# Kernel optimization log

Hardware: AMD Instinct MI355X
Metric: run time of the kernel (lower is better)

Reference implementation:

```python
import jax, jax.numpy as jnp
import numpy as np

B, S, D, H = 4, 2048, 768, 12
DEPTH = D // H


def setup_inputs() -> dict:
    key = jax.random.key(0)
    ks = jax.random.split(key, 8)
    scale = 1.0 / np.sqrt(D)
    return {
        "v": jax.random.normal(ks[0], (B, S, D), jnp.float32),
        "k": jax.random.normal(ks[1], (B, S, D), jnp.float32),
        "q": jax.random.normal(ks[2], (B, S, D), jnp.float32),
        "wq": jax.random.normal(ks[3], (D, D), jnp.float32) * scale,
        "wk": jax.random.normal(ks[4], (D, D), jnp.float32) * scale,
        "wv": jax.random.normal(ks[5], (D, D), jnp.float32) * scale,
        "wo": jax.random.normal(ks[6], (D, D), jnp.float32) * scale,
        "bo": jax.random.normal(ks[7], (D,), jnp.float32) * 0.01,
    }


def _split_heads(x):
    # [B, S, D] -> [B, H, S, depth]
    return x.reshape(B, S, H, DEPTH).transpose(0, 2, 1, 3)


def reference(v, k, q, wq, wk, wv, wo, bo):
    # nn.Linear(bias=False): y = x @ W.T
    qh = _split_heads(q @ wq.T)
    kh = _split_heads(k @ wk.T)
    vh = _split_heads(v @ wv.T)
    # scaled dot-product attention (mask=None)
    logits = jnp.einsum("bhqd,bhkd->bhqk", qh, kh) / jnp.sqrt(
        jnp.asarray(DEPTH, jnp.float32)
    )
    attn = jax.nn.softmax(logits, axis=-1)  # [B, H, Sq, Sk]
    out = jnp.einsum("bhqk,bhkd->bhqd", attn, vh)
    concat = out.transpose(0, 2, 1, 3).reshape(B, S, D)
    return concat @ wo.T + bo
```

## Files before the change

kernel.cpp:

```cpp
#include <hip/hip_runtime.h>
#include <math.h>

#define BB 4
#define SS 2048
#define DD 768
#define HH 12
#define DEPTH 64
#define M_TOTAL (BB * SS)
#define WSZ (DD * DD)

typedef __attribute__((ext_vector_type(8))) short bf16x8;
typedef __attribute__((ext_vector_type(16))) float f32x16;
typedef __attribute__((ext_vector_type(4))) float f32x4;
typedef __attribute__((ext_vector_type(4))) unsigned short us4;
typedef __attribute__((ext_vector_type(2))) unsigned int u32x2;
typedef __attribute__((ext_vector_type(4))) unsigned int u32x4;

__device__ __forceinline__ unsigned short f2b(float f) {
  unsigned u = __builtin_bit_cast(unsigned, f);
  return (unsigned short)((u + 0x8000u) >> 16);
}

__device__ __forceinline__ unsigned pkrnd(float lo, float hi) {
  unsigned a = __builtin_bit_cast(unsigned, lo) + 0x8000u;
  unsigned b = __builtin_bit_cast(unsigned, hi) + 0x8000u;
  return __builtin_amdgcn_perm(b, a, 0x07060302);
}

__device__ __forceinline__ us4 f2b4(float a, float b, float c, float d) {
  unsigned lo = pkrnd(a, b), hi = pkrnd(c, d);
  us4 t;
  t.x = (unsigned short)lo; t.y = (unsigned short)(lo >> 16);
  t.z = (unsigned short)hi; t.w = (unsigned short)(hi >> 16);
  return t;
}

__device__ __forceinline__ float fexp2(float x) {
  return __builtin_amdgcn_exp2f(x);
}

#if __has_builtin(__builtin_amdgcn_permlane32_swap)
__device__ __forceinline__ void plswap(unsigned& a, unsigned& b) {
  u32x2 r = __builtin_amdgcn_permlane32_swap(a, b, false, false);
  a = r.x;
  b = r.y;
}
#else
__device__ __forceinline__ void plswap(unsigned& a, unsigned& b) {
  unsigned pa = (unsigned)__shfl_xor((int)a, 32, 64);
  unsigned pb = (unsigned)__shfl_xor((int)b, 32, 64);
  bool hi = ((threadIdx.x & 63) >> 5) != 0;
  unsigned na = hi ? pb : a;
  unsigned nb = hi ? b : pa;
  a = na;
  b = nb;
}
#endif

__device__ __forceinline__ void gl16(const void* g, void* l) {
  __builtin_amdgcn_global_load_lds(
      (const __attribute__((address_space(1))) unsigned int*)g,
      (__attribute__((address_space(3))) unsigned int*)l, 16, 0, 0);
}

__global__ __launch_bounds__(256) void prep(
    const float* __restrict__ s0, const float* __restrict__ s1,
    const float* __restrict__ s2, const float* __restrict__ s3,
    const float* __restrict__ s4, const float* __restrict__ s5,
    const float* __restrict__ s6, unsigned short* __restrict__ d0,
    unsigned short* __restrict__ d1, unsigned short* __restrict__ d2,
    unsigned short* __restrict__ d3, unsigned short* __restrict__ d4,
    unsigned short* __restrict__ d5, unsigned short* __restrict__ d6) {
  const float* s;
  unsigned short* d;
  int n;
  switch (blockIdx.y) {
    case 0: s = s0; d = d0; n = M_TOTAL * DD; break;
    case 1: s = s1; d = d1; n = M_TOTAL * DD; break;
    case 2: s = s2; d = d2; n = M_TOTAL * DD; break;
    case 3: s = s3; d = d3; n = WSZ; break;
    case 4: s = s4; d = d4; n = WSZ; break;
    case 5: s = s5; d = d5; n = WSZ; break;
    default: s = s6; d = d6; n = WSZ; break;
  }
  int idx = (blockIdx.x * 256 + threadIdx.x) * 4;
  if (idx >= n) return;
  float4 f = *(const float4*)(s + idx);
  *(us4*)(d + idx) = f2b4(f.x, f.y, f.z, f.w);
}

__global__ __launch_bounds__(256) void proj_qkv(
    const unsigned short* __restrict__ qb, const unsigned short* __restrict__ kb,
    const unsigned short* __restrict__ vb, const unsigned short* __restrict__ wqb,
    const unsigned short* __restrict__ wkb, const unsigned short* __restrict__ wvb,
    unsigned short* __restrict__ QF, unsigned short* __restrict__ KF,
    unsigned short* __restrict__ VF) {
  const int mode = blockIdx.z;
  const unsigned short* X;
  const unsigned short* W;
  if (mode == 0) { X = qb; W = wqb; }
  else if (mode == 1) { X = kb; W = wkb; }
  else { X = vb; W = wvb; }

  __shared__ __align__(16) char sm[34816];
  unsigned short* As = (unsigned short*)sm;
  unsigned short* Bs = (unsigned short*)(sm + 8192);
  unsigned short* Ts = (unsigned short*)sm;

  const int tid = threadIdx.x;
  const int lane = tid & 63, w_ = tid >> 6;
  const int lr = lane & 15, quad = lane >> 4;
  const int wm = (w_ & 1) * 64, wn = (w_ >> 1) * 64;
  const int m0 = blockIdx.x * 128, n0 = blockIdx.y * 128;
  const int grow = lane >> 2, gcol = (lane & 3) * 8;

  f32x4 acc[4][4];
#pragma unroll
  for (int mt = 0; mt < 4; ++mt)
#pragma unroll
    for (int nt = 0; nt < 4; ++nt) acc[mt][nt] = (f32x4){0.f, 0.f, 0.f, 0.f};

  for (int k0 = 0; k0 < DD; k0 += 32) {
    __syncthreads();
#pragma unroll
    for (int i = 0; i < 2; ++i) {
      int c = 4 * i + w_;
      int row = c * 16 + grow;
      gl16(X + (size_t)(m0 + row) * DD + k0 + gcol, (char*)As + c * 1024);
      gl16(W + (size_t)(n0 + row) * DD + k0 + gcol, (char*)Bs + c * 1024);
    }
    __syncthreads();

    bf16x8 af[4];
#pragma unroll
    for (int mt = 0; mt < 4; ++mt)
      af[mt] = *(const bf16x8*)&As[(wm + 16 * mt + lr) * 32 + 8 * quad];
#pragma unroll
    for (int nt = 0; nt < 4; ++nt) {
      bf16x8 bf = *(const bf16x8*)&Bs[(wn + 16 * nt + lr) * 32 + 8 * quad];
#pragma unroll
      for (int mt = 0; mt < 4; ++mt)
        acc[mt][nt] = __builtin_amdgcn_mfma_f32_16x16x32_bf16(af[mt], bf,
                                                              acc[mt][nt], 0, 0, 0);
    }
  }

  __syncthreads();

  const int b_ = m0 >> 11;
  const int hbase = n0 >> 6;
  const int sgbase = (m0 & 2047) >> 5;

  if (mode < 2) {
    const float osc = (mode == 0) ? 0.18033688011f : 1.0f;
#pragma unroll
    for (int mt = 0; mt < 4; ++mt)
#pragma unroll
      for (int nt = 0; nt < 4; ++nt) {
        int n = wn + 16 * nt + lr;
        int mb = wm + 16 * mt + 4 * quad;
#pragma unroll
        for (int r = 0; r < 4; ++r)
          Ts[(mb + r) * 136 + n] = f2b(acc[mt][nt][r] * osc);
      }
    __syncthreads();
    unsigned short* O = (mode == 0) ? QF : KF;
    const int ks = tid >> 6, lane2 = tid & 63;
    const int mrow = lane2 & 31, hb = lane2 >> 5;
#pragma unroll
    for (int c = 0; c < 8; ++c) {
      int hl = c >> 2, sblk = c & 3;
      int bh = b_ * HH + hbase + hl;
      bf16x8 vv = *(const bf16x8*)&Ts[(sblk * 32 + mrow) * 136 + hl * 64 +
                                      ks * 16 + hb * 8];
      *(bf16x8*)(O + ((size_t)bh * 64 + sgbase + sblk) * 2048 + tid * 8) = vv;
    }
  } else {
#pragma unroll
    for (int mt = 0; mt < 4; ++mt)
#pragma unroll
      for (int nt = 0; nt < 4; ++nt) {
        int n = wn + 16 * nt + lr;
        int mb = wm + 16 * mt + 4 * quad;
        *(us4*)&Ts[n * 136 + mb] =
            f2b4(acc[mt][nt][0], acc[mt][nt][1], acc[mt][nt][2], acc[mt][nt][3]);
      }
    __syncthreads();
    const int ntv = tid >> 7, ks2 = (tid >> 6) & 1, lane2 = tid & 63;
#pragma unroll
    for (int c = 0; c < 8; ++c) {
      int hl = c >> 2, sblk = c & 3;
      int bh = b_ * HH + hbase + hl;
      bf16x8 vv = *(const bf16x8*)&Ts[(hl * 64 + ntv * 32 + (lane2 & 31)) * 136 +
                                      sblk * 32 + ks2 * 16 + (lane2 >> 5) * 8];
      *(bf16x8*)(VF + ((size_t)bh * 64 + sgbase + sblk) * 2048 + tid * 8) = vv;
    }
  }
}

struct KV {
  bf16x8 k[4];
  bf16x8 v[4];
};

__global__ __launch_bounds__(256) void attn(
    const unsigned short* __restrict__ QF, const unsigned short* __restrict__ KF,
    const unsigned short* __restrict__ VF, unsigned short* __restrict__ cc) {
  __shared__ __align__(16) char smem[19200];
  float (*Osh)[64][36] = (float (*)[64][36])smem;
  float (*Ls)[2][32] = (float (*)[2][32])(smem + 18432);
  float (*Linv)[32] = (float (*)[32])(smem + 18944);

  const int tid = threadIdx.x;
  const int lane = tid & 63, w_ = tid >> 6;
  const int wq = w_ & 1, wk = w_ >> 1;
  const int m32 = lane & 31, h = lane >> 5;
  const int bh = blockIdx.x % 48;
  const int q0 = (blockIdx.x / 48) * 64;
  const size_t perbh = (size_t)SS * DEPTH;

  const unsigned short* qfb = QF + (size_t)bh * perbh;
  const unsigned short* kfb = KF + (size_t)bh * perbh + (size_t)wk * 2048 + lane * 8;
  const unsigned short* vfb = VF + (size_t)bh * perbh + (size_t)wk * 2048 + lane * 8;

  bf16x8 qf[4];
  {
    const unsigned short* p = qfb + (size_t)((q0 >> 5) + wq) * 2048 + lane * 8;
#pragma unroll
    for (int ks = 0; ks < 4; ++ks) qf[ks] = *(const bf16x8*)(p + ks * 512);
  }

  f32x16 o[2];
#pragma unroll
  for (int nt = 0; nt < 2; ++nt)
#pragma unroll
    for (int r = 0; r < 16; ++r) o[nt][r] = 0.f;
  float l_lane = 0.f;

#define LOADKV(tile, dst)                                                    \
  do {                                                                       \
    const unsigned short* kp_ = kfb + (size_t)(tile) * 4096;                 \
    const unsigned short* vp_ = vfb + (size_t)(tile) * 4096;                 \
    _Pragma("unroll") for (int x_ = 0; x_ < 4; ++x_) {                       \
      (dst).k[x_] = *(const bf16x8*)(kp_ + x_ * 512);                        \
      (dst).v[x_] = *(const bf16x8*)(vp_ + x_ * 512);                        \
    }                                                                        \
  } while (0)

#define TILECOMP(kv)                                                         \
  do {                                                                       \
    f32x16 st;                                                               \
    _Pragma("unroll") for (int r_ = 0; r_ < 16; ++r_) st[r_] = 0.f;          \
    _Pragma("unroll") for (int ks_ = 0; ks_ < 4; ++ks_)                      \
        st = __builtin_amdgcn_mfma_f32_32x32x16_bf16((kv).k[ks_], qf[ks_],   \
                                                     st, 0, 0, 0);           \
    float e_[16];                                                            \
    _Pragma("unroll") for (int r_ = 0; r_ < 16; ++r_) {                      \
      e_[r_] = fexp2(st[r_]);                                                \
      l_lane += e_[r_];                                                      \
    }                                                                        \
    unsigned p_[8];                                                          \
    _Pragma("unroll") for (int g_ = 0; g_ < 8; ++g_)                         \
        p_[g_] = pkrnd(e_[2 * g_], e_[2 * g_ + 1]);                          \
    plswap(p_[0], p_[2]);                                                    \
    plswap(p_[1], p_[3]);                                                    \
    plswap(p_[4], p_[6]);                                                    \
    plswap(p_[5], p_[7]);                                                    \
    u32x4 fa_ = {p_[0], p_[1], p_[2], p_[3]};                                \
    u32x4 fb_ = {p_[4], p_[5], p_[6], p_[7]};                                \
    bf16x8 pa1 = __builtin_bit_cast(bf16x8, fa_);                            \
    bf16x8 pa2 = __builtin_bit_cast(bf16x8, fb_);                            \
    o[0] = __builtin_amdgcn_mfma_f32_32x32x16_bf16(pa1, (kv).v[0], o[0], 0, 0, 0); \
    o[1] = __builtin_amdgcn_mfma_f32_32x32x16_bf16(pa1, (kv).v[2], o[1], 0, 0, 0); \
    o[0] = __builtin_amdgcn_mfma_f32_32x32x16_bf16(pa2, (kv).v[1], o[0], 0, 0, 0); \
    o[1] = __builtin_amdgcn_mfma_f32_32x32x16_bf16(pa2, (kv).v[3], o[1], 0, 0, 0); \
  } while (0)

  KV b0, b1;
  LOADKV(0, b0);
  for (int t = 0; t < 32; t += 2) {
    LOADKV(t + 1, b1);
    TILECOMP(b0);
    if (t + 2 < 32) LOADKV(t + 2, b0);
    TILECOMP(b1);
  }

  l_lane += __shfl_xor(l_lane, 32);
  if (h == 0) Ls[wq][wk][m32] = l_lane;
  __syncthreads();
  if (wk == 1) {
#pragma unroll
    for (int nt = 0; nt < 2; ++nt)
#pragma unroll
      for (int g = 0; g < 4; ++g) {
        float4 t = make_float4(o[nt][4 * g], o[nt][4 * g + 1], o[nt][4 * g + 2],
                               o[nt][4 * g + 3]);
        *(float4*)&Osh[wq][32 * nt + m32][8 * g + 4 * h] = t;
      }
  } else if (tid < 64) {
    int qq = tid & 31, ww = tid >> 5;
    Linv[ww][qq] = 1.f / (Ls[ww][0][qq] + Ls[ww][1][qq]);
  }
  __syncthreads();
  if (wk == 0) {
    const int b_ = bh / HH, h_ = bh % HH;
#pragma unroll
    for (int g = 0; g < 4; ++g) {
      float4 li = *(const float4*)&Linv[wq][8 * g + 4 * h];
      float lia[4] = {li.x, li.y, li.z, li.w};
#pragma unroll
      for (int nt = 0; nt < 2; ++nt) {
        float4 ot = *(const float4*)&Osh[wq][32 * nt + m32][8 * g + 4 * h];
        float oa[4] = {ot.x, ot.y, ot.z, ot.w};
#pragma unroll
        for (int r = 0; r < 4; ++r) {
          int qg = q0 + 32 * wq + 8 * g + 4 * h + r;
          float val = (o[nt][4 * g + r] + oa[r]) * lia[r];
          cc[((size_t)b_ * SS + qg) * DD + h_ * DEPTH + 32 * nt + m32] = f2b(val);
        }
      }
    }
  }
}

__global__ __launch_bounds__(256) void proj_out(
    const unsigned short* __restrict__ cc, const unsigned short* __restrict__ wob,
    const float* __restrict__ bo, float* __restrict__ out) {
  __shared__ __align__(16) unsigned short As[128 * 32];
  __shared__ __align__(16) unsigned short Bs[128 * 32];

  const int tid = threadIdx.x;
  const int lane = tid & 63, w_ = tid >> 6;
  const int lr = lane & 15, quad = lane >> 4;
  const int wm = (w_ & 1) * 64, wn = (w_ >> 1) * 64;
  const int m0 = blockIdx.x * 128, n0 = blockIdx.y * 128;
  const int grow = lane >> 2, gcol = (lane & 3) * 8;

  f32x4 acc[4][4];
#pragma unroll
  for (int mt = 0; mt < 4; ++mt)
#pragma unroll
    for (int nt = 0; nt < 4; ++nt) acc[mt][nt] = (f32x4){0.f, 0.f, 0.f, 0.f};

  for (int k0 = 0; k0 < DD; k0 += 32) {
    __syncthreads();
#pragma unroll
    for (int i = 0; i < 2; ++i) {
      int c = 4 * i + w_;
      int row = c * 16 + grow;
      gl16(cc + (size_t)(m0 + row) * DD + k0 + gcol, (char*)As + c * 1024);
      gl16(wob + (size_t)(n0 + row) * DD + k0 + gcol, (char*)Bs + c * 1024);
    }
    __syncthreads();

    bf16x8 af[4];
#pragma unroll
    for (int mt = 0; mt < 4; ++mt)
      af[mt] = *(const bf16x8*)&As[(wm + 16 * mt + lr) * 32 + 8 * quad];
#pragma unroll
    for (int nt = 0; nt < 4; ++nt) {
      bf16x8 bf = *(const bf16x8*)&Bs[(wn + 16 * nt + lr) * 32 + 8 * quad];
#pragma unroll
      for (int mt = 0; mt < 4; ++mt)
        acc[mt][nt] = __builtin_amdgcn_mfma_f32_16x16x32_bf16(af[mt], bf,
                                                              acc[mt][nt], 0, 0, 0);
    }
  }

#pragma unroll
  for (int mt = 0; mt < 4; ++mt)
#pragma unroll
    for (int nt = 0; nt < 4; ++nt) {
      int n = n0 + wn + 16 * nt + lr;
      float bias = bo[n];
#pragma unroll
      for (int r = 0; r < 4; ++r) {
        int m = m0 + wm + 16 * mt + 4 * quad + r;
        out[(size_t)m * DD + n] = acc[mt][nt][r] + bias;
      }
    }
}

extern "C" void kernel_launch(void* const* d_in, const int* in_sizes, int n_in,
                              void* d_out, int out_size, void* d_ws,
                              size_t ws_size, hipStream_t stream) {
  const float* v = (const float*)d_in[0];
  const float* k = (const float*)d_in[1];
  const float* q = (const float*)d_in[2];
  const float* wq = (const float*)d_in[3];
  const float* wk = (const float*)d_in[4];
  const float* wv = (const float*)d_in[5];
  const float* wo = (const float*)d_in[6];
  const float* bo = (const float*)d_in[7];
  float* out = (float*)d_out;

  const size_t per = (size_t)BB * HH * SS * DEPTH;
  unsigned short* QF = (unsigned short*)d_ws;
  unsigned short* KF = QF + per;
  unsigned short* VF = KF + per;
  unsigned short* cc = VF + per;
  unsigned short* qb = cc + per;
  unsigned short* kb = qb + per;
  unsigned short* vb = kb + per;
  unsigned short* wqb = vb + per;
  unsigned short* wkb = wqb + WSZ;
  unsigned short* wvb = wkb + WSZ;
  unsigned short* wob = wvb + WSZ;

  dim3 g0(M_TOTAL * DD / 1024, 7);
  prep<<<g0, 256, 0, stream>>>(q, k, v, wq, wk, wv, wo, qb, kb, vb, wqb, wkb,
                               wvb, wob);

  dim3 g1(M_TOTAL / 128, DD / 128, 3);
  proj_qkv<<<g1, 256, 0, stream>>>(qb, kb, vb, wqb, wkb, wvb, QF, KF, VF);

  attn<<<dim3(48 * (SS / 64)), 256, 0, stream>>>(QF, KF, VF, cc);

  dim3 g3(M_TOTAL / 128, DD / 128);
  proj_out<<<g3, 256, 0, stream>>>(cc, wob, bo, out);
}
```

Baseline: 276.3 us.

## Reuse each K/V tile across two query blocks per wave in attention

The attention kernel drops from four waves (2 query × 2 key splits) to two waves per block. Each wave now holds two 32-row query fragments and reuses every loaded K/V tile for both, halving K/V global loads per query. The cost is more accumulator registers per wave and fewer waves per block to hide latency. Separately, the prep conversion kernel becomes grid-stride with one launch row for all four weight matrices instead of many mostly-idle blocks.

```diff
diff --git a/kernel.cpp b/kernel.cpp
--- a/kernel.cpp
+++ b/kernel.cpp
@@ -69,24 +69,27 @@
     const float* __restrict__ s4, const float* __restrict__ s5,
     const float* __restrict__ s6, unsigned short* __restrict__ d0,
     unsigned short* __restrict__ d1, unsigned short* __restrict__ d2,
-    unsigned short* __restrict__ d3, unsigned short* __restrict__ d4,
-    unsigned short* __restrict__ d5, unsigned short* __restrict__ d6) {
-  const float* s;
-  unsigned short* d;
-  int n;
-  switch (blockIdx.y) {
-    case 0: s = s0; d = d0; n = M_TOTAL * DD; break;
-    case 1: s = s1; d = d1; n = M_TOTAL * DD; break;
-    case 2: s = s2; d = d2; n = M_TOTAL * DD; break;
-    case 3: s = s3; d = d3; n = WSZ; break;
-    case 4: s = s4; d = d4; n = WSZ; break;
-    case 5: s = s5; d = d5; n = WSZ; break;
-    default: s = s6; d = d6; n = WSZ; break;
-  }
-  int idx = (blockIdx.x * 256 + threadIdx.x) * 4;
-  if (idx >= n) return;
-  float4 f = *(const float4*)(s + idx);
-  *(us4*)(d + idx) = f2b4(f.x, f.y, f.z, f.w);
+    unsigned short* __restrict__ dw) {
+  const int y = blockIdx.y;
+  const int stride = gridDim.x * 256 * 4;
+  if (y < 3) {
+    const float* s = (y == 0) ? s0 : (y == 1) ? s1 : s2;
+    unsigned short* d = (y == 0) ? d0 : (y == 1) ? d1 : d2;
+    for (int idx = (blockIdx.x * 256 + threadIdx.x) * 4; idx < M_TOTAL * DD;
+         idx += stride) {
+      float4 f = *(const float4*)(s + idx);
+      *(us4*)(d + idx) = f2b4(f.x, f.y, f.z, f.w);
+    }
+  } else {
+    for (int idx = (blockIdx.x * 256 + threadIdx.x) * 4; idx < 4 * WSZ;
+         idx += stride) {
+      int wi = idx / WSZ;
+      int off = idx - wi * WSZ;
+      const float* s = (wi == 0) ? s3 : (wi == 1) ? s4 : (wi == 2) ? s5 : s6;
+      float4 f = *(const float4*)(s + off);
+      *(us4*)(dw + idx) = f2b4(f.x, f.y, f.z, f.w);
+    }
+  }
 }
 
 __global__ __launch_bounds__(256) void proj_qkv(
@@ -203,39 +206,41 @@
   bf16x8 v[4];
 };
 
-__global__ __launch_bounds__(256) void attn(
+__global__ __launch_bounds__(128) void attn(
     const unsigned short* __restrict__ QF, const unsigned short* __restrict__ KF,
     const unsigned short* __restrict__ VF, unsigned short* __restrict__ cc) {
-  __shared__ __align__(16) char smem[19200];
-  float (*Osh)[64][36] = (float (*)[64][36])smem;
-  float (*Ls)[2][32] = (float (*)[2][32])(smem + 18432);
-  float (*Linv)[32] = (float (*)[32])(smem + 18944);
+  __shared__ __align__(16) float Osh[64][68];
+  __shared__ float Ls[2][2][32];
+  __shared__ float Linv[2][32];
 
   const int tid = threadIdx.x;
   const int lane = tid & 63, w_ = tid >> 6;
-  const int wq = w_ & 1, wk = w_ >> 1;
   const int m32 = lane & 31, h = lane >> 5;
   const int bh = blockIdx.x % 48;
-  const int q0 = (blockIdx.x / 48) * 64;
+  const int qi = blockIdx.x / 48;
+  const int q0 = qi * 64;
   const size_t perbh = (size_t)SS * DEPTH;
 
   const unsigned short* qfb = QF + (size_t)bh * perbh;
-  const unsigned short* kfb = KF + (size_t)bh * perbh + (size_t)wk * 2048 + lane * 8;
-  const unsigned short* vfb = VF + (size_t)bh * perbh + (size_t)wk * 2048 + lane * 8;
-
-  bf16x8 qf[4];
-  {
-    const unsigned short* p = qfb + (size_t)((q0 >> 5) + wq) * 2048 + lane * 8;
-#pragma unroll
-    for (int ks = 0; ks < 4; ++ks) qf[ks] = *(const bf16x8*)(p + ks * 512);
-  }
-
-  f32x16 o[2];
-#pragma unroll
-  for (int nt = 0; nt < 2; ++nt)
-#pragma unroll
-    for (int r = 0; r < 16; ++r) o[nt][r] = 0.f;
-  float l_lane = 0.f;
+  const unsigned short* kfb =
+      KF + (size_t)bh * perbh + (size_t)w_ * 2048 + lane * 8;
+  const unsigned short* vfb =
+      VF + (size_t)bh * perbh + (size_t)w_ * 2048 + lane * 8;
+
+  bf16x8 qf[2][4];
+#pragma unroll
+  for (int g = 0; g < 2; ++g)
+#pragma unroll
+    for (int x = 0; x < 4; ++x)
+      qf[g][x] = *(const bf16x8*)(qfb + (size_t)(2 * qi + g) * 2048 + x * 512 +
+                                  lane * 8);
+
+  f32x16 o[4];
+#pragma unroll
+  for (int i = 0; i < 4; ++i)
+#pragma unroll
+    for (int r = 0; r < 16; ++r) o[i][r] = 0.f;
+  float l0 = 0.f, l1 = 0.f;
 
 #define LOADKV(tile, dst)                                                    \
   do {                                                                       \
@@ -247,79 +252,104 @@
     }                                                                        \
   } while (0)
 
-#define TILECOMP(kv)                                                         \
+#define TILE(kv)                                                             \
   do {                                                                       \
-    f32x16 st;                                                               \
-    _Pragma("unroll") for (int r_ = 0; r_ < 16; ++r_) st[r_] = 0.f;          \
-    _Pragma("unroll") for (int ks_ = 0; ks_ < 4; ++ks_)                      \
-        st = __builtin_amdgcn_mfma_f32_32x32x16_bf16((kv).k[ks_], qf[ks_],   \
-                                                     st, 0, 0, 0);           \
-    float e_[16];                                                            \
+    f32x16 s0, s1;                                                           \
     _Pragma("unroll") for (int r_ = 0; r_ < 16; ++r_) {                      \
-      e_[r_] = fexp2(st[r_]);                                                \
-      l_lane += e_[r_];                                                      \
+      s0[r_] = 0.f;                                                          \
+      s1[r_] = 0.f;                                                          \
     }                                                                        \
-    unsigned p_[8];                                                          \
-    _Pragma("unroll") for (int g_ = 0; g_ < 8; ++g_)                         \
-        p_[g_] = pkrnd(e_[2 * g_], e_[2 * g_ + 1]);                          \
-    plswap(p_[0], p_[2]);                                                    \
-    plswap(p_[1], p_[3]);                                                    \
-    plswap(p_[4], p_[6]);                                                    \
-    plswap(p_[5], p_[7]);                                                    \
-    u32x4 fa_ = {p_[0], p_[1], p_[2], p_[3]};                                \
-    u32x4 fb_ = {p_[4], p_[5], p_[6], p_[7]};                                \
-    bf16x8 pa1 = __builtin_bit_cast(bf16x8, fa_);                            \
-    bf16x8 pa2 = __builtin_bit_cast(bf16x8, fb_);                            \
-    o[0] = __builtin_amdgcn_mfma_f32_32x32x16_bf16(pa1, (kv).v[0], o[0], 0, 0, 0); \
-    o[1] = __builtin_amdgcn_mfma_f32_32x32x16_bf16(pa1, (kv).v[2], o[1], 0, 0, 0); \
-    o[0] = __builtin_amdgcn_mfma_f32_32x32x16_bf16(pa2, (kv).v[1], o[0], 0, 0, 0); \
-    o[1] = __builtin_amdgcn_mfma_f32_32x32x16_bf16(pa2, (kv).v[3], o[1], 0, 0, 0); \
+    _Pragma("unroll") for (int x_ = 0; x_ < 4; ++x_) {                       \
+      s0 = __builtin_amdgcn_mfma_f32_32x32x16_bf16((kv).k[x_], qf[0][x_],    \
+                                                   s0, 0, 0, 0);             \
+      s1 = __builtin_amdgcn_mfma_f32_32x32x16_bf16((kv).k[x_], qf[1][x_],    \
+                                                   s1, 0, 0, 0);             \
+    }                                                                        \
+    unsigned p0[8], p1[8];                                                   \
+    _Pragma("unroll") for (int rr_ = 0; rr_ < 8; ++rr_) {                    \
+      float a0_ = fexp2(s0[2 * rr_]), a1_ = fexp2(s0[2 * rr_ + 1]);          \
+      float b0_ = fexp2(s1[2 * rr_]), b1_ = fexp2(s1[2 * rr_ + 1]);          \
+      l0 += a0_ + a1_;                                                       \
+      l1 += b0_ + b1_;                                                       \
+      p0[rr_] = pkrnd(a0_, a1_);                                             \
+      p1[rr_] = pkrnd(b0_, b1_);                                             \
+    }                                                                        \
+    plswap(p0[0], p0[2]); plswap(p0[1], p0[3]);                              \
+    plswap(p0[4], p0[6]); plswap(p0[5], p0[7]);                              \
+    plswap(p1[0], p1[2]); plswap(p1[1], p1[3]);                              \
+    plswap(p1[4], p1[6]); plswap(p1[5], p1[7]);                              \
+    u32x4 fa0_ = {p0[0], p0[1], p0[2], p0[3]};                               \
+    u32x4 fb0_ = {p0[4], p0[5], p0[6], p0[7]};                               \
+    u32x4 fa1_ = {p1[0], p1[1], p1[2], p1[3]};                               \
+    u32x4 fb1_ = {p1[4], p1[5], p1[6], p1[7]};                               \
+    bf16x8 q00_ = __builtin_bit_cast(bf16x8, fa0_);                          \
+    bf16x8 q01_ = __builtin_bit_cast(bf16x8, fb0_);                          \
+    bf16x8 q10_ = __builtin_bit_cast(bf16x8, fa1_);                          \
+    bf16x8 q11_ = __builtin_bit_cast(bf16x8, fb1_);                          \
+    o[0] = __builtin_amdgcn_mfma_f32_32x32x16_bf16(q00_, (kv).v[0], o[0], 0, 0, 0); \
+    o[1] = __builtin_amdgcn_mfma_f32_32x32x16_bf16(q00_, (kv).v[2], o[1], 0, 0, 0); \
+    o[2] = __builtin_amdgcn_mfma_f32_32x32x16_bf16(q10_, (kv).v[0], o[2], 0, 0, 0); \
+    o[3] = __builtin_amdgcn_mfma_f32_32x32x16_bf16(q10_, (kv).v[2], o[3], 0, 0, 0); \
+    o[0] = __builtin_amdgcn_mfma_f32_32x32x16_bf16(q01_, (kv).v[1], o[0], 0, 0, 0); \
+    o[1] = __builtin_amdgcn_mfma_f32_32x32x16_bf16(q01_, (kv).v[3], o[1], 0, 0, 0); \
+    o[2] = __builtin_amdgcn_mfma_f32_32x32x16_bf16(q11_, (kv).v[1], o[2], 0, 0, 0); \
+    o[3] = __builtin_amdgcn_mfma_f32_32x32x16_bf16(q11_, (kv).v[3], o[3], 0, 0, 0); \
   } while (0)
 
   KV b0, b1;
   LOADKV(0, b0);
   for (int t = 0; t < 32; t += 2) {
     LOADKV(t + 1, b1);
-    TILECOMP(b0);
+    TILE(b0);
     if (t + 2 < 32) LOADKV(t + 2, b0);
-    TILECOMP(b1);
-  }
-
-  l_lane += __shfl_xor(l_lane, 32);
-  if (h == 0) Ls[wq][wk][m32] = l_lane;
+    TILE(b1);
+  }
+
+  l0 += __shfl_xor(l0, 32);
+  l1 += __shfl_xor(l1, 32);
+  if (h == 0) {
+    Ls[w_][0][m32] = l0;
+    Ls[w_][1][m32] = l1;
+  }
+  if (w_ == 1) {
+#pragma unroll
+    for (int g = 0; g < 2; ++g)
+#pragma unroll
+      for (int nt = 0; nt < 2; ++nt)
+#pragma unroll
+        for (int rr = 0; rr < 4; ++rr) {
+          float4 t = make_float4(o[2 * g + nt][4 * rr], o[2 * g + nt][4 * rr + 1],
+                                 o[2 * g + nt][4 * rr + 2],
+                                 o[2 * g + nt][4 * rr + 3]);
+          *(float4*)&Osh[32 * nt + m32][32 * g + 8 * rr + 4 * h] = t;
+        }
+  }
   __syncthreads();
-  if (wk == 1) {
-#pragma unroll
-    for (int nt = 0; nt < 2; ++nt)
-#pragma unroll
-      for (int g = 0; g < 4; ++g) {
-        float4 t = make_float4(o[nt][4 * g], o[nt][4 * g + 1], o[nt][4 * g + 2],
-                               o[nt][4 * g + 3]);
-        *(float4*)&Osh[wq][32 * nt + m32][8 * g + 4 * h] = t;
-      }
-  } else if (tid < 64) {
-    int qq = tid & 31, ww = tid >> 5;
-    Linv[ww][qq] = 1.f / (Ls[ww][0][qq] + Ls[ww][1][qq]);
-  }
-  __syncthreads();
-  if (wk == 0) {
+  if (w_ == 0) {
+    {
+      int g = tid >> 5, q = tid & 31;
+      Linv[g][q] = 1.f / (Ls[0][g][q] + Ls[1][g][q]);
+    }
     const int b_ = bh / HH, h_ = bh % HH;
 #pragma unroll
-    for (int g = 0; g < 4; ++g) {
-      float4 li = *(const float4*)&Linv[wq][8 * g + 4 * h];
-      float lia[4] = {li.x, li.y, li.z, li.w};
-#pragma unroll
-      for (int nt = 0; nt < 2; ++nt) {
-        float4 ot = *(const float4*)&Osh[wq][32 * nt + m32][8 * g + 4 * h];
-        float oa[4] = {ot.x, ot.y, ot.z, ot.w};
-#pragma unroll
-        for (int r = 0; r < 4; ++r) {
-          int qg = q0 + 32 * wq + 8 * g + 4 * h + r;
-          float val = (o[nt][4 * g + r] + oa[r]) * lia[r];
-          cc[((size_t)b_ * SS + qg) * DD + h_ * DEPTH + 32 * nt + m32] = f2b(val);
+    for (int g = 0; g < 2; ++g)
+#pragma unroll
+      for (int rr = 0; rr < 4; ++rr) {
+        float4 li = *(const float4*)&Linv[g][8 * rr + 4 * h];
+        float lia[4] = {li.x, li.y, li.z, li.w};
+#pragma unroll
+        for (int nt = 0; nt < 2; ++nt) {
+          float4 ot = *(const float4*)&Osh[32 * nt + m32][32 * g + 8 * rr + 4 * h];
+          float oa[4] = {ot.x, ot.y, ot.z, ot.w};
+#pragma unroll
+          for (int r = 0; r < 4; ++r) {
+            int qg = q0 + 32 * g + 8 * rr + 4 * h + r;
+            float val = (o[2 * g + nt][4 * rr + r] + oa[r]) * lia[r];
+            cc[((size_t)b_ * SS + qg) * DD + h_ * DEPTH + 32 * nt + m32] =
+                f2b(val);
+          }
         }
       }
-    }
   }
 }
 
@@ -407,14 +437,13 @@
   unsigned short* wvb = wkb + WSZ;
   unsigned short* wob = wvb + WSZ;
 
-  dim3 g0(M_TOTAL * DD / 1024, 7);
-  prep<<<g0, 256, 0, stream>>>(q, k, v, wq, wk, wv, wo, qb, kb, vb, wqb, wkb,
-                               wvb, wob);
+  dim3 g0(1536, 4);
+  prep<<<g0, 256, 0, stream>>>(q, k, v, wq, wk, wv, wo, qb, kb, vb, wqb);
 
   dim3 g1(M_TOTAL / 128, DD / 128, 3);
   proj_qkv<<<g1, 256, 0, stream>>>(qb, kb, vb, wqb, wkb, wvb, QF, KF, VF);
 
-  attn<<<dim3(48 * (SS / 64)), 256, 0, stream>>>(QF, KF, VF, cc);
+  attn<<<dim3(48 * (SS / 64)), 128, 0, stream>>>(QF, KF, VF, cc);
 
   dim3 g3(M_TOTAL / 128, DD / 128);
   proj_out<<<g3, 256, 0, stream>>>(cc, wob, bo, out);
```

Measured after the change: 277.7 us. About the same (+0.5%).
